# Performance work log

Hardware: AMD Instinct MI355X
Metric: run time of the kernel (lower is better)

## Reference

```python
import jax, jax.numpy as jnp
import numpy as np

B, IN, H, OUT, N = 2048, 512, 512, 256, 32768

def setup_inputs() -> dict:
    key = jax.random.key(0)
    ks = jax.random.split(key, 12)
    s = 1.0 / np.sqrt(H)
    inp = {
        'x': jax.random.normal(ks[0], (B, IN), jnp.float32),
        'Wih0': jax.random.uniform(ks[1], (3 * H, IN), jnp.float32, -s, s),
        'Whh0': jax.random.uniform(ks[2], (3 * H, H), jnp.float32, -s, s),
        'bih0': jax.random.uniform(ks[3], (3 * H,), jnp.float32, -s, s),
        'bhh0': jax.random.uniform(ks[4], (3 * H,), jnp.float32, -s, s),
        'Wih1': jax.random.uniform(ks[5], (3 * H, H), jnp.float32, -s, s),
        'Whh1': jax.random.uniform(ks[6], (3 * H, H), jnp.float32, -s, s),
        'bih1': jax.random.uniform(ks[7], (3 * H,), jnp.float32, -s, s),
        'bhh1': jax.random.uniform(ks[8], (3 * H,), jnp.float32, -s, s),
        'Wout': jax.random.uniform(ks[9], (OUT, H), jnp.float32, -s, s),
        'bout': jax.random.uniform(ks[10], (OUT,), jnp.float32, -s, s),
        'pre_set_idx': jnp.sort(jax.random.randint(ks[11], (N,), 0, B)),
    }
    return inp


def _gru_layer(seq, Wih, Whh, bih, bhh):
    # seq: [B, T, D]; PyTorch GRU gate order: r, z, n
    h_dim = Whh.shape[1]
    xp = jnp.einsum('btd,gd->btg', seq, Wih) + bih  # [B, T, 3H]
    xr, xz, xn = jnp.split(xp, 3, axis=-1)
    Whr, Whz, Whn = jnp.split(Whh, 3, axis=0)
    bhr, bhz, bhn = jnp.split(bhh, 3)

    def step(h, xs):
        xr_t, xz_t, xn_t = xs
        r = jax.nn.sigmoid(xr_t + h @ Whr.T + bhr)
        z = jax.nn.sigmoid(xz_t + h @ Whz.T + bhz)
        n = jnp.tanh(xn_t + r * (h @ Whn.T + bhn))
        h_new = (1.0 - z) * n + z * h
        return h_new, h_new

    h0 = jnp.zeros((seq.shape[0], h_dim), seq.dtype)
    xs = (xr.transpose(1, 0, 2), xz.transpose(1, 0, 2), xn.transpose(1, 0, 2))
    _, ys = jax.lax.scan(step, h0, xs)  # ys: [T, B, H]
    return ys.transpose(1, 0, 2)


def reference(x, Wih0, Whh0, bih0, bhh0, Wih1, Whh1, bih1, bhh1, Wout, bout, pre_set_idx):
    psi_np = np.asarray(pre_set_idx)
    counts_np = np.bincount(psi_np, minlength=B)
    T = int(counts_np.max())  # scipy mode(...).count == max count (static w.r.t. seed)

    # replicate the single-step input T times (original cat loop)
    x_seq = jnp.broadcast_to(x[:, None, :], (B, T, x.shape[1]))
    y0 = _gru_layer(x_seq, Wih0, Whh0, bih0, bhh0)
    y1 = _gru_layer(y0, Wih1, Whh1, bih1, bhh1)  # [B, T, H]

    # masked gather: for batch i, keep first cnt[i] timesteps (pre_set_idx is sorted)
    counts = jnp.asarray(counts_np)
    starts = jnp.concatenate([jnp.zeros(1, counts.dtype), jnp.cumsum(counts)[:-1]])
    rank = jnp.arange(N) - starts[pre_set_idx]  # position within each group
    gather_idx = pre_set_idx * T + rank
    flat = y1.reshape(-1, H)  # [B*T, H]
    sel = flat[gather_idx]  # [N, H]
    return sel @ Wout.T + bout  # [N, OUT]
```

## Files before the change

### kernel.cpp

```cpp
#include <hip/hip_runtime.h>
#include <math.h>

#define Bn   2048
#define Hd   512
#define H3   1536
#define OUTD 256
#define Nn   32768
#define TMAX 48
#define Kd   512

typedef __attribute__((ext_vector_type(8))) short short8v;
typedef __attribute__((ext_vector_type(4))) float float4v;

__device__ __forceinline__ float sigm(float x) { return 1.0f / (1.0f + __expf(-x)); }

__device__ __forceinline__ short f2bf(float v) {
    union { float f; unsigned u; } a; a.f = v;
    unsigned r = a.u + 0x7fffu + ((a.u >> 16) & 1u);
    return (short)(r >> 16);
}
__device__ __forceinline__ float bf2f(short s) {
    union { float f; unsigned u; } a; a.u = ((unsigned)(unsigned short)s) << 16;
    return a.f;
}

#define MF(acc, A, B) acc = __builtin_amdgcn_mfma_f32_16x16x32_bf16(A, B, acc, 0, 0, 0)

__global__ void prologue(const int* __restrict__ psi, int* __restrict__ perm,
                         int* __restrict__ startsP, int* __restrict__ active) {
    __shared__ int hist[64];
    __shared__ int base[64];
    __shared__ int cur[64];
    __shared__ int cnt_s[Bn];
    __shared__ int start_s[Bn];
    const int tid = threadIdx.x;
    if (tid < 64) { hist[tid] = 0; cur[tid] = 0; }
    __syncthreads();
    for (int b = tid; b < Bn; b += 1024) {
        int lo = 0, hi = Nn;
        while (lo < hi) { int mid = (lo + hi) >> 1; if (psi[mid] < b) lo = mid + 1; else hi = mid; }
        int lb = lo;
        lo = 0; hi = Nn;
        while (lo < hi) { int mid = (lo + hi) >> 1; if (psi[mid] <= b) lo = mid + 1; else hi = mid; }
        int c = lo - lb;
        cnt_s[b] = c;
        start_s[b] = lb;
        atomicAdd(&hist[min(c, 63)], 1);
    }
    __syncthreads();
    if (tid == 0) {
        base[63] = 0;
        for (int c = 62; c >= 0; --c) base[c] = base[c + 1] + hist[c + 1];
    }
    __syncthreads();
    if (tid < 64) active[tid] = base[tid];
    for (int b = tid; b < Bn; b += 1024) {
        int c = min(cnt_s[b], 63);
        int pos = base[c] + atomicAdd(&cur[c], 1);
        perm[pos] = b;
        startsP[pos] = start_s[b];
    }
}

__global__ __launch_bounds__(256)
void split_kern(const float* __restrict__ src, short* __restrict__ hi,
                short* __restrict__ lo, int n) {
    int i = (blockIdx.x * 256 + threadIdx.x) * 4;
    if (i >= n) return;
    float4 v = *(const float4*)&src[i];
    float vv[4] = {v.x, v.y, v.z, v.w};
    short h4[4], l4[4];
    #pragma unroll
    for (int c = 0; c < 4; ++c) {
        short h = f2bf(vv[c]);
        h4[c] = h;
        l4[c] = f2bf(vv[c] - bf2f(h));
    }
    *(short4*)&hi[i] = make_short4(h4[0], h4[1], h4[2], h4[3]);
    *(short4*)&lo[i] = make_short4(l4[0], l4[1], l4[2], l4[3]);
}

__global__ __launch_bounds__(256)
void split_perm(const float* __restrict__ src, const int* __restrict__ perm,
                short* __restrict__ hi, short* __restrict__ lo) {
    int i = (blockIdx.x * 256 + threadIdx.x) * 4;
    int row = i >> 9, col = i & 511;
    int srow = perm[row];
    float4 v = *(const float4*)&src[(size_t)srow * 512 + col];
    float vv[4] = {v.x, v.y, v.z, v.w};
    short h4[4], l4[4];
    #pragma unroll
    for (int c = 0; c < 4; ++c) {
        short h = f2bf(vv[c]);
        h4[c] = h;
        l4[c] = f2bf(vv[c] - bf2f(h));
    }
    *(short4*)&hi[i] = make_short4(h4[0], h4[1], h4[2], h4[3]);
    *(short4*)&lo[i] = make_short4(l4[0], l4[1], l4[2], l4[3]);
}

__global__ __launch_bounds__(256)
void pack_w1rz(const float* __restrict__ Wih1, const float* __restrict__ Whh1,
               short* __restrict__ hi, short* __restrict__ lo) {
    int i = (blockIdx.x * 256 + threadIdx.x) * 4;
    int orow = i >> 10, k = i & 1023;
    const float* s = (k < 512) ? &Wih1[(size_t)orow * 512 + k]
                               : &Whh1[(size_t)orow * 512 + (k - 512)];
    float4 v = *(const float4*)s;
    float vv[4] = {v.x, v.y, v.z, v.w};
    short h4[4], l4[4];
    #pragma unroll
    for (int c = 0; c < 4; ++c) {
        short h = f2bf(vv[c]);
        h4[c] = h;
        l4[c] = f2bf(vv[c] - bf2f(h));
    }
    *(short4*)&hi[i] = make_short4(h4[0], h4[1], h4[2], h4[3]);
    *(short4*)&lo[i] = make_short4(l4[0], l4[1], l4[2], l4[3]);
}

__global__ __launch_bounds__(256)
void zero4(short* __restrict__ a, short* __restrict__ b,
           short* __restrict__ c, short* __restrict__ d, int n) {
    int i = (blockIdx.x * 256 + threadIdx.x) * 4;
    if (i >= n) return;
    short4 z = make_short4(0, 0, 0, 0);
    *(short4*)&a[i] = z; *(short4*)&b[i] = z;
    *(short4*)&c[i] = z; *(short4*)&d[i] = z;
}

template<bool SPLIT_A>
__device__ __forceinline__ void gemm_tile(
    const short* __restrict__ Ahi, const short* __restrict__ Alo,
    const short* __restrict__ Whi, const short* __restrict__ Wlo,
    const float* __restrict__ bias, float* __restrict__ C,
    int m0, int n0, int ldC, short* lds) {
    short* ldsAhi = lds;
    short* ldsAlo = lds + 4096;
    short* ldsBhi = lds + 8192;
    short* ldsBlo = lds + 12288;
    const int tid = threadIdx.x;
    const int wid = tid >> 6, lane = tid & 63;
    const int wm = wid >> 1, wn = wid & 1;
    const int oi0 = tid * 2, oi1 = tid * 2 + 1;
    const int r0 = oi0 >> 2, c0 = oi0 & 3;
    const int r1 = oi1 >> 2, c1 = oi1 & 3;
    const int w0 = ((r0 >> 4) * 64 + (r0 & 15) + (c0 << 4)) * 8;
    const int w1 = ((r1 >> 4) * 64 + (r1 & 15) + (c1 << 4)) * 8;

    float4v acc[4][4] = {};
    int4 ah0, ah1, al0, al1, bh0, bh1, bl0, bl1;

#define LOADK(kt) do { const int k0 = (kt) * 32; \
    ah0 = *(const int4*)&Ahi[(size_t)(m0 + r0) * Kd + k0 + c0 * 8]; \
    ah1 = *(const int4*)&Ahi[(size_t)(m0 + r1) * Kd + k0 + c1 * 8]; \
    if constexpr (SPLIT_A) { \
        al0 = *(const int4*)&Alo[(size_t)(m0 + r0) * Kd + k0 + c0 * 8]; \
        al1 = *(const int4*)&Alo[(size_t)(m0 + r1) * Kd + k0 + c1 * 8]; } \
    bh0 = *(const int4*)&Whi[(size_t)(n0 + r0) * Kd + k0 + c0 * 8]; \
    bh1 = *(const int4*)&Whi[(size_t)(n0 + r1) * Kd + k0 + c1 * 8]; \
    bl0 = *(const int4*)&Wlo[(size_t)(n0 + r0) * Kd + k0 + c0 * 8]; \
    bl1 = *(const int4*)&Wlo[(size_t)(n0 + r1) * Kd + k0 + c1 * 8]; } while (0)

    LOADK(0);
    for (int kt = 0; kt < 16; ++kt) {
        __syncthreads();
        *(int4*)&ldsAhi[w0] = ah0; *(int4*)&ldsAhi[w1] = ah1;
        if constexpr (SPLIT_A) { *(int4*)&ldsAlo[w0] = al0; *(int4*)&ldsAlo[w1] = al1; }
        *(int4*)&ldsBhi[w0] = bh0; *(int4*)&ldsBhi[w1] = bh1;
        *(int4*)&ldsBlo[w0] = bl0; *(int4*)&ldsBlo[w1] = bl1;
        __syncthreads();
        if (kt < 15) LOADK(kt + 1);
        short8v afh[4], afl[4], bfh[4], bfl[4];
        #pragma unroll
        for (int mi = 0; mi < 4; ++mi) {
            afh[mi] = *(const short8v*)&ldsAhi[((wm * 4 + mi) * 64 + lane) * 8];
            if constexpr (SPLIT_A)
                afl[mi] = *(const short8v*)&ldsAlo[((wm * 4 + mi) * 64 + lane) * 8];
        }
        #pragma unroll
        for (int ni = 0; ni < 4; ++ni) {
            bfh[ni] = *(const short8v*)&ldsBhi[((wn * 4 + ni) * 64 + lane) * 8];
            bfl[ni] = *(const short8v*)&ldsBlo[((wn * 4 + ni) * 64 + lane) * 8];
        }
        #pragma unroll
        for (int mi = 0; mi < 4; ++mi)
            #pragma unroll
            for (int ni = 0; ni < 4; ++ni) {
                MF(acc[mi][ni], afh[mi], bfh[ni]);
                MF(acc[mi][ni], afh[mi], bfl[ni]);
                if constexpr (SPLIT_A) MF(acc[mi][ni], afl[mi], bfh[ni]);
            }
    }
#undef LOADK
    #pragma unroll
    for (int mi = 0; mi < 4; ++mi) {
        #pragma unroll
        for (int ni = 0; ni < 4; ++ni) {
            int row = m0 + wm * 64 + mi * 16 + ((lane >> 4) << 2);
            int col = n0 + wn * 64 + ni * 16 + (lane & 15);
            float bv = bias ? bias[col] : 0.0f;
            #pragma unroll
            for (int r = 0; r < 4; ++r)
                C[(size_t)(row + r) * ldC + col] = acc[mi][ni][r] + bv;
        }
    }
}

template<bool SPLIT_A>
__global__ __launch_bounds__(256)
void gemm_one(const short* __restrict__ Ahi, const short* __restrict__ Alo,
              const short* __restrict__ Whi, const short* __restrict__ Wlo,
              const float* __restrict__ bias, float* __restrict__ C, int ntn) {
    __shared__ short lds[16384];
    int m0 = (blockIdx.x / ntn) * 128, n0 = (blockIdx.x % ntn) * 128;
    gemm_tile<SPLIT_A>(Ahi, Alo, Whi, Wlo, bias, C, m0, n0, ntn * 128, lds);
}

__global__ __launch_bounds__(256)
void fused_step(const short* __restrict__ OLDhi, const short* __restrict__ OLDlo,
                short* __restrict__ NEWhi, short* __restrict__ NEWlo,
                const short* __restrict__ W0hi, const short* __restrict__ W0lo,
                const short* __restrict__ Wrzhi, const short* __restrict__ Wrzlo,
                const short* __restrict__ Wnxhi, const short* __restrict__ Wnxlo,
                const short* __restrict__ Wnhhi, const short* __restrict__ Wnhlo,
                const float* __restrict__ xp0P, const float* __restrict__ bhh0,
                const float* __restrict__ bih1, const float* __restrict__ bhh1,
                short* __restrict__ sel_h, const int* __restrict__ startsP,
                const int* __restrict__ active, int i) {
    __shared__ short lds[14336];
    const int tid = threadIdx.x;
    const int bb = blockIdx.x;
    const int part = (bb >= 256);
    const int idx = bb & 255;
    const int js = idx >> 4, mb = idx & 15;
    const int m0 = mb * 128, j0 = js * 32;
    const int wid = tid >> 6, lane = tid & 63;
    const int wm = wid >> 1, wn = wid & 1;

    short* ldsAhi = lds;
    short* ldsAlo = lds + 4096;
    short* ldsP   = lds + 8192;

    const int oiA0 = tid * 2, oiA1 = tid * 2 + 1;
    const int rA0 = oiA0 >> 2, cA0 = oiA0 & 3;
    const int rA1 = oiA1 >> 2, cA1 = oiA1 & 3;
    const int wA0 = ((rA0 >> 4) * 64 + (rA0 & 15) + (cA0 << 4)) * 8;
    const int wA1 = ((rA1 >> 4) * 64 + (rA1 & 15) + (cA1 << 4)) * 8;

    const short* aB0h = OLDhi + (size_t)(m0 + rA0) * 1024 + cA0 * 8;
    const short* aB1h = OLDhi + (size_t)(m0 + rA1) * 1024 + cA1 * 8;
    const short* aB0l = OLDlo + (size_t)(m0 + rA0) * 1024 + cA0 * 8;
    const short* aB1l = OLDlo + (size_t)(m0 + rA1) * 1024 + cA1 * 8;

    int wPq[3], pg[3], prw[3], poc[3];
    #pragma unroll
    for (int rep = 0; rep < 3; ++rep) {
        int id2 = rep * 256 + tid;
        int p = id2 >> 7, wi = id2 & 127;
        int prow = wi >> 2, poct = wi & 3;
        wPq[rep] = p * 1024 + ((prow >> 4) * 64 + (prow & 15) + (poct << 4)) * 8;
        pg[rep] = p; prw[rep] = prow; poc[rep] = poct;
    }

    const int col = j0 + wn * 16 + (lane & 15);

#define AFRAGS \
    short8v afh[4], afl[4]; \
    _Pragma("unroll") for (int mi = 0; mi < 4; ++mi) { \
        afh[mi] = *(const short8v*)&ldsAhi[((wm * 4 + mi) * 64 + lane) * 8]; \
        afl[mi] = *(const short8v*)&ldsAlo[((wm * 4 + mi) * 64 + lane) * 8]; }

#define GATEB(ACC, G) { \
    short8v bh = *(const short8v*)&ldsP[((G) * 2 + 0) * 1024 + (wn * 64 + lane) * 8]; \
    short8v bl = *(const short8v*)&ldsP[((G) * 2 + 1) * 1024 + (wn * 64 + lane) * 8]; \
    _Pragma("unroll") for (int mi = 0; mi < 4; ++mi) { \
        MF(ACC[mi], afh[mi], bh); MF(ACC[mi], afh[mi], bl); MF(ACC[mi], afl[mi], bh); } }

    if (part == 0) {
        const int act = active[i];
        if (m0 >= act) return;
        const short* pb[3];
        #pragma unroll
        for (int rep = 0; rep < 3; ++rep) {
            const short* W = (pg[rep] & 1) ? W0lo : W0hi;
            pb[rep] = W + (size_t)((pg[rep] >> 1) * 512 + j0 + prw[rep]) * 512 + poc[rep] * 8;
        }
        float4v aR[4] = {}, aZ[4] = {}, aN[4] = {};
        int4 s0, s1, s2, s3, q0, q1, q2;
        auto LOAD = [&](int kt) {
            int k0 = kt * 32;
            s0 = *(const int4*)(aB0h + k0); s1 = *(const int4*)(aB1h + k0);
            s2 = *(const int4*)(aB0l + k0); s3 = *(const int4*)(aB1l + k0);
            q0 = *(const int4*)(pb[0] + k0);
            q1 = *(const int4*)(pb[1] + k0);
            q2 = *(const int4*)(pb[2] + k0);
        };
        LOAD(0);
        for (int kt = 0; kt < 16; ++kt) {
            __syncthreads();
            *(int4*)&ldsAhi[wA0] = s0; *(int4*)&ldsAhi[wA1] = s1;
            *(int4*)&ldsAlo[wA0] = s2; *(int4*)&ldsAlo[wA1] = s3;
            *(int4*)&ldsP[wPq[0]] = q0; *(int4*)&ldsP[wPq[1]] = q1; *(int4*)&ldsP[wPq[2]] = q2;
            __syncthreads();
            if (kt < 15) LOAD(kt + 1);
            AFRAGS
            GATEB(aR, 0)
            GATEB(aZ, 1)
            GATEB(aN, 2)
        }
        const float b_r = bhh0[col], b_z = bhh0[512 + col], b_n = bhh0[1024 + col];
        #pragma unroll
        for (int mi = 0; mi < 4; ++mi) {
            int rowb = m0 + wm * 64 + mi * 16 + ((lane >> 4) << 2);
            #pragma unroll
            for (int r = 0; r < 4; ++r) {
                int row = rowb + r;
                float xr = xp0P[(size_t)row * H3 + col];
                float xz = xp0P[(size_t)row * H3 + 512 + col];
                float xn = xp0P[(size_t)row * H3 + 1024 + col];
                float rr = sigm(xr + aR[mi][r] + b_r);
                float zz = sigm(xz + aZ[mi][r] + b_z);
                float nn = tanhf(xn + rr * (aN[mi][r] + b_n));
                float hp = bf2f(OLDhi[(size_t)row * 1024 + col]) + bf2f(OLDlo[(size_t)row * 1024 + col]);
                float h = (1.0f - zz) * nn + zz * hp;
                short hh = f2bf(h);
                NEWhi[(size_t)row * 1024 + col] = hh;
                NEWlo[(size_t)row * 1024 + col] = f2bf(h - bf2f(hh));
            }
        }
    } else {
        if (i < 1) return;
        const int act = active[i - 1];
        if (m0 >= act) return;
        const int t = i - 1;
        const short* pbRZ[3]; const short* pbNx[3]; const short* pbNh[3]; int isn[3];
        #pragma unroll
        for (int rep = 0; rep < 3; ++rep) {
            int g = pg[rep] >> 1, hl = pg[rep] & 1;
            isn[rep] = (g == 2);
            const short* Wrz = hl ? Wrzlo : Wrzhi;
            const short* Wx  = hl ? Wnxlo : Wnxhi;
            const short* Wh  = hl ? Wnhlo : Wnhhi;
            pbRZ[rep] = Wrz + (size_t)(min(g, 1) * 512 + j0 + prw[rep]) * 1024 + poc[rep] * 8;
            pbNx[rep] = Wx + (size_t)(j0 + prw[rep]) * 512 + poc[rep] * 8;
            pbNh[rep] = Wh + (size_t)(j0 + prw[rep]) * 512 + poc[rep] * 8;
        }
        float4v aR[4] = {}, aZ[4] = {}, aXn[4] = {}, aHn[4] = {};
        int4 s0, s1, s2, s3, q0, q1, q2;
        auto LOAD = [&](int kt) {
            int k0 = kt * 32;
            s0 = *(const int4*)(aB0h + k0); s1 = *(const int4*)(aB1h + k0);
            s2 = *(const int4*)(aB0l + k0); s3 = *(const int4*)(aB1l + k0);
            q0 = *(const int4*)(isn[0] ? ((kt < 16) ? pbNx[0] + k0 : pbNh[0] + (k0 - 512)) : pbRZ[0] + k0);
            q1 = *(const int4*)(isn[1] ? ((kt < 16) ? pbNx[1] + k0 : pbNh[1] + (k0 - 512)) : pbRZ[1] + k0);
            q2 = *(const int4*)(isn[2] ? ((kt < 16) ? pbNx[2] + k0 : pbNh[2] + (k0 - 512)) : pbRZ[2] + k0);
        };
        LOAD(0);
        for (int kt = 0; kt < 16; ++kt) {
            __syncthreads();
            *(int4*)&ldsAhi[wA0] = s0; *(int4*)&ldsAhi[wA1] = s1;
            *(int4*)&ldsAlo[wA0] = s2; *(int4*)&ldsAlo[wA1] = s3;
            *(int4*)&ldsP[wPq[0]] = q0; *(int4*)&ldsP[wPq[1]] = q1; *(int4*)&ldsP[wPq[2]] = q2;
            __syncthreads();
            LOAD(kt + 1);
            AFRAGS
            GATEB(aR, 0)
            GATEB(aZ, 1)
            GATEB(aXn, 2)
        }
        for (int kt = 16; kt < 32; ++kt) {
            __syncthreads();
            *(int4*)&ldsAhi[wA0] = s0; *(int4*)&ldsAhi[wA1] = s1;
            *(int4*)&ldsAlo[wA0] = s2; *(int4*)&ldsAlo[wA1] = s3;
            *(int4*)&ldsP[wPq[0]] = q0; *(int4*)&ldsP[wPq[1]] = q1; *(int4*)&ldsP[wPq[2]] = q2;
            __syncthreads();
            if (kt < 31) LOAD(kt + 1);
            AFRAGS
            GATEB(aR, 0)
            GATEB(aZ, 1)
            GATEB(aHn, 2)
        }
        const float b_r = bih1[col] + bhh1[col];
        const float b_z = bih1[512 + col] + bhh1[512 + col];
        const float b_xn = bih1[1024 + col];
        const float b_hn = bhh1[1024 + col];
        #pragma unroll
        for (int mi = 0; mi < 4; ++mi) {
            int rowb = m0 + wm * 64 + mi * 16 + ((lane >> 4) << 2);
            #pragma unroll
            for (int r = 0; r < 4; ++r) {
                int row = rowb + r;
                float rr = sigm(aR[mi][r] + b_r);
                float zz = sigm(aZ[mi][r] + b_z);
                float nn = tanhf(aXn[mi][r] + b_xn + rr * (aHn[mi][r] + b_hn));
                float hp = bf2f(OLDhi[(size_t)row * 1024 + 512 + col]) + bf2f(OLDlo[(size_t)row * 1024 + 512 + col]);
                float h = (1.0f - zz) * nn + zz * hp;
                short hh = f2bf(h);
                NEWhi[(size_t)row * 1024 + 512 + col] = hh;
                NEWlo[(size_t)row * 1024 + 512 + col] = f2bf(h - bf2f(hh));
                if (row < act)
                    sel_h[((size_t)startsP[row] + t) * Hd + col] = f2bf(h);
            }
        }
    }
#undef AFRAGS
#undef GATEB
}

extern "C" void kernel_launch(void* const* d_in, const int* in_sizes, int n_in,
                              void* d_out, int out_size, void* d_ws, size_t ws_size,
                              hipStream_t stream) {
    (void)in_sizes; (void)n_in; (void)out_size; (void)ws_size;
    const float* x    = (const float*)d_in[0];
    const float* Wih0 = (const float*)d_in[1];
    const float* Whh0 = (const float*)d_in[2];
    const float* bih0 = (const float*)d_in[3];
    const float* bhh0 = (const float*)d_in[4];
    const float* Wih1 = (const float*)d_in[5];
    const float* Whh1 = (const float*)d_in[6];
    const float* bih1 = (const float*)d_in[7];
    const float* bhh1 = (const float*)d_in[8];
    const float* Wout = (const float*)d_in[9];
    const float* bout = (const float*)d_in[10];
    const int*   psi  = (const int*)d_in[11];
    float* out = (float*)d_out;

    char* p = (char*)d_ws;
    auto alloc = [&](size_t bytes) { char* r = p; p += (bytes + 255) & ~255ULL; return r; };
    short* xPhi   = (short*)alloc((size_t)Bn * Kd * 2);
    short* xPlo   = (short*)alloc((size_t)Bn * Kd * 2);
    short* Wih0hi = (short*)alloc((size_t)H3 * Kd * 2);
    short* Wih0lo = (short*)alloc((size_t)H3 * Kd * 2);
    short* W0hi   = (short*)alloc((size_t)H3 * Kd * 2);
    short* W0lo   = (short*)alloc((size_t)H3 * Kd * 2);
    short* Wrzhi  = (short*)alloc((size_t)1024 * 1024 * 2);
    short* Wrzlo  = (short*)alloc((size_t)1024 * 1024 * 2);
    short* Wnxhi  = (short*)alloc((size_t)512 * 512 * 2);
    short* Wnxlo  = (short*)alloc((size_t)512 * 512 * 2);
    short* Wnhhi  = (short*)alloc((size_t)512 * 512 * 2);
    short* Wnhlo  = (short*)alloc((size_t)512 * 512 * 2);
    short* Wouthi = (short*)alloc((size_t)OUTD * Kd * 2);
    short* Woutlo = (short*)alloc((size_t)OUTD * Kd * 2);
    float* xp0P   = (float*)alloc((size_t)Bn * H3 * 4);
    short* Aahi   = (short*)alloc((size_t)Bn * 1024 * 2);
    short* Aalo   = (short*)alloc((size_t)Bn * 1024 * 2);
    short* Abhi   = (short*)alloc((size_t)Bn * 1024 * 2);
    short* Ablo   = (short*)alloc((size_t)Bn * 1024 * 2);
    short* sel_h  = (short*)alloc((size_t)Nn * Hd * 2);
    int* perm     = (int*)alloc(Bn * 4);
    int* startsP  = (int*)alloc(Bn * 4);
    int* active   = (int*)alloc(64 * 4);

    prologue<<<1, 1024, 0, stream>>>(psi, perm, startsP, active);
    split_perm<<<1024, 256, 0, stream>>>(x, perm, xPhi, xPlo);
    split_kern<<<768, 256, 0, stream>>>(Wih0, Wih0hi, Wih0lo, H3 * Kd);
    split_kern<<<768, 256, 0, stream>>>(Whh0, W0hi, W0lo, H3 * Kd);
    pack_w1rz<<<1024, 256, 0, stream>>>(Wih1, Whh1, Wrzhi, Wrzlo);
    split_kern<<<256, 256, 0, stream>>>(Wih1 + (size_t)1024 * 512, Wnxhi, Wnxlo, 512 * 512);
    split_kern<<<256, 256, 0, stream>>>(Whh1 + (size_t)1024 * 512, Wnhhi, Wnhlo, 512 * 512);
    split_kern<<<128, 256, 0, stream>>>(Wout, Wouthi, Woutlo, OUTD * Kd);
    zero4<<<2048, 256, 0, stream>>>(Aahi, Aalo, Abhi, Ablo, Bn * 1024);

    gemm_one<true><<<192, 256, 0, stream>>>(xPhi, xPlo, Wih0hi, Wih0lo, bih0, xp0P, 12);

    for (int i = 0; i <= TMAX; ++i) {
        const short* OLDhi = (i & 1) ? Abhi : Aahi;
        const short* OLDlo = (i & 1) ? Ablo : Aalo;
        short* NEWhi = (i & 1) ? Aahi : Abhi;
        short* NEWlo = (i & 1) ? Aalo : Ablo;
        fused_step<<<512, 256, 0, stream>>>(OLDhi, OLDlo, NEWhi, NEWlo,
                                            W0hi, W0lo, Wrzhi, Wrzlo,
                                            Wnxhi, Wnxlo, Wnhhi, Wnhlo,
                                            xp0P, bhh0, bih1, bhh1,
                                            sel_h, startsP, active, i);
    }

    gemm_one<false><<<512, 256, 0, stream>>>(sel_h, nullptr, Wouthi, Woutlo, bout, out, 2);
}
```

Before: 1.766 ms.

## Rebalance fused GRU step tiles: wider layer-0 N tiles, smaller layer-1 M tiles

Layer-0 blocks now compute 128x64 output tiles (128 blocks) instead of 128x32 (256 blocks), which halves redundant reloads of the hidden-state A tile. Layer-1 blocks use 64x64 tiles (256 blocks), so the longer K=1024 work is split across more blocks and the two layers are better balanced. The grid drops from 512 to 384 blocks, LDS grows to 40KB, and launch bounds request 2 blocks per CU. This trades per-block register pressure and LDS use for less redundant global loading and better load balance.

Result: slower. 4.008 ms (+127.0%).

```diff
diff --git a/kernel.cpp b/kernel.cpp
--- a/kernel.cpp
+++ b/kernel.cpp
@@ -217,7 +217,7 @@
     gemm_tile<SPLIT_A>(Ahi, Alo, Whi, Wlo, bias, C, m0, n0, ntn * 128, lds);
 }
 
-__global__ __launch_bounds__(256)
+__global__ __launch_bounds__(256, 2)
 void fused_step(const short* __restrict__ OLDhi, const short* __restrict__ OLDlo,
                 short* __restrict__ NEWhi, short* __restrict__ NEWlo,
                 const short* __restrict__ W0hi, const short* __restrict__ W0lo,
@@ -228,184 +228,218 @@
                 const float* __restrict__ bih1, const float* __restrict__ bhh1,
                 short* __restrict__ sel_h, const int* __restrict__ startsP,
                 const int* __restrict__ active, int i) {
-    __shared__ short lds[14336];
+    __shared__ short lds[20480];
+    short* ldsA = lds;
+    short* ldsP = lds + 8192;
     const int tid = threadIdx.x;
     const int bb = blockIdx.x;
-    const int part = (bb >= 256);
-    const int idx = bb & 255;
-    const int js = idx >> 4, mb = idx & 15;
-    const int m0 = mb * 128, j0 = js * 32;
     const int wid = tid >> 6, lane = tid & 63;
     const int wm = wid >> 1, wn = wid & 1;
 
-    short* ldsAhi = lds;
-    short* ldsAlo = lds + 4096;
-    short* ldsP   = lds + 8192;
-
-    const int oiA0 = tid * 2, oiA1 = tid * 2 + 1;
-    const int rA0 = oiA0 >> 2, cA0 = oiA0 & 3;
-    const int rA1 = oiA1 >> 2, cA1 = oiA1 & 3;
-    const int wA0 = ((rA0 >> 4) * 64 + (rA0 & 15) + (cA0 << 4)) * 8;
-    const int wA1 = ((rA1 >> 4) * 64 + (rA1 & 15) + (cA1 << 4)) * 8;
-
-    const short* aB0h = OLDhi + (size_t)(m0 + rA0) * 1024 + cA0 * 8;
-    const short* aB1h = OLDhi + (size_t)(m0 + rA1) * 1024 + cA1 * 8;
-    const short* aB0l = OLDlo + (size_t)(m0 + rA0) * 1024 + cA0 * 8;
-    const short* aB1l = OLDlo + (size_t)(m0 + rA1) * 1024 + cA1 * 8;
-
-    int wPq[3], pg[3], prw[3], poc[3];
-    #pragma unroll
-    for (int rep = 0; rep < 3; ++rep) {
-        int id2 = rep * 256 + tid;
-        int p = id2 >> 7, wi = id2 & 127;
-        int prow = wi >> 2, poct = wi & 3;
-        wPq[rep] = p * 1024 + ((prow >> 4) * 64 + (prow & 15) + (poct << 4)) * 8;
-        pg[rep] = p; prw[rep] = prow; poc[rep] = poct;
-    }
-
-    const int col = j0 + wn * 16 + (lane & 15);
-
-#define AFRAGS \
-    short8v afh[4], afl[4]; \
-    _Pragma("unroll") for (int mi = 0; mi < 4; ++mi) { \
-        afh[mi] = *(const short8v*)&ldsAhi[((wm * 4 + mi) * 64 + lane) * 8]; \
-        afl[mi] = *(const short8v*)&ldsAlo[((wm * 4 + mi) * 64 + lane) * 8]; }
-
-#define GATEB(ACC, G) { \
-    short8v bh = *(const short8v*)&ldsP[((G) * 2 + 0) * 1024 + (wn * 64 + lane) * 8]; \
-    short8v bl = *(const short8v*)&ldsP[((G) * 2 + 1) * 1024 + (wn * 64 + lane) * 8]; \
-    _Pragma("unroll") for (int mi = 0; mi < 4; ++mi) { \
-        MF(ACC[mi], afh[mi], bh); MF(ACC[mi], afh[mi], bl); MF(ACC[mi], afl[mi], bh); } }
-
-    if (part == 0) {
+    if (bb < 128) {
         const int act = active[i];
+        const int mb = bb >> 3, js = bb & 7;
+        const int m0 = mb * 128, j0 = js * 64;
         if (m0 >= act) return;
-        const short* pb[3];
-        #pragma unroll
-        for (int rep = 0; rep < 3; ++rep) {
-            const short* W = (pg[rep] & 1) ? W0lo : W0hi;
-            pb[rep] = W + (size_t)((pg[rep] >> 1) * 512 + j0 + prw[rep]) * 512 + poc[rep] * 8;
-        }
-        float4v aR[4] = {}, aZ[4] = {}, aN[4] = {};
-        int4 s0, s1, s2, s3, q0, q1, q2;
+
+        int aOff[4]; const short* aSrc[4];
+        #pragma unroll
+        for (int rep = 0; rep < 4; ++rep) {
+            int u = rep * 256 + tid;
+            int half = u >> 9, wi = u & 511;
+            int ar = wi >> 2, ac = wi & 3;
+            aOff[rep] = half * 4096 + ((ar >> 4) * 64 + (ar & 15) + (ac << 4)) * 8;
+            aSrc[rep] = (half ? OLDlo : OLDhi) + (size_t)(m0 + ar) * 1024 + ac * 8;
+        }
+        int pOff[6]; const short* pSrc[6];
+        #pragma unroll
+        for (int rep = 0; rep < 6; ++rep) {
+            int u = rep * 256 + tid;
+            int p = u >> 8, wi = u & 255;
+            int pr = wi >> 2, pc = wi & 3;
+            pOff[rep] = p * 2048 + ((pr >> 4) * 64 + (pr & 15) + (pc << 4)) * 8;
+            int g = p >> 1, hl = p & 1;
+            pSrc[rep] = (hl ? W0lo : W0hi) + (size_t)(g * 512 + j0 + pr) * 512 + pc * 8;
+        }
+
+        float4v aR[4][2] = {}, aZ[4][2] = {}, aN[4][2] = {};
+        int4 av[4], pv[6];
         auto LOAD = [&](int kt) {
-            int k0 = kt * 32;
-            s0 = *(const int4*)(aB0h + k0); s1 = *(const int4*)(aB1h + k0);
-            s2 = *(const int4*)(aB0l + k0); s3 = *(const int4*)(aB1l + k0);
-            q0 = *(const int4*)(pb[0] + k0);
-            q1 = *(const int4*)(pb[1] + k0);
-            q2 = *(const int4*)(pb[2] + k0);
+            const int k0 = kt * 32;
+            #pragma unroll
+            for (int rep = 0; rep < 4; ++rep) av[rep] = *(const int4*)(aSrc[rep] + k0);
+            #pragma unroll
+            for (int rep = 0; rep < 6; ++rep) pv[rep] = *(const int4*)(pSrc[rep] + k0);
         };
         LOAD(0);
         for (int kt = 0; kt < 16; ++kt) {
             __syncthreads();
-            *(int4*)&ldsAhi[wA0] = s0; *(int4*)&ldsAhi[wA1] = s1;
-            *(int4*)&ldsAlo[wA0] = s2; *(int4*)&ldsAlo[wA1] = s3;
-            *(int4*)&ldsP[wPq[0]] = q0; *(int4*)&ldsP[wPq[1]] = q1; *(int4*)&ldsP[wPq[2]] = q2;
+            #pragma unroll
+            for (int rep = 0; rep < 4; ++rep) *(int4*)&ldsA[aOff[rep]] = av[rep];
+            #pragma unroll
+            for (int rep = 0; rep < 6; ++rep) *(int4*)&ldsP[pOff[rep]] = pv[rep];
             __syncthreads();
             if (kt < 15) LOAD(kt + 1);
-            AFRAGS
-            GATEB(aR, 0)
-            GATEB(aZ, 1)
-            GATEB(aN, 2)
-        }
-        const float b_r = bhh0[col], b_z = bhh0[512 + col], b_n = bhh0[1024 + col];
-        #pragma unroll
-        for (int mi = 0; mi < 4; ++mi) {
-            int rowb = m0 + wm * 64 + mi * 16 + ((lane >> 4) << 2);
-            #pragma unroll
-            for (int r = 0; r < 4; ++r) {
-                int row = rowb + r;
-                float xr = xp0P[(size_t)row * H3 + col];
-                float xz = xp0P[(size_t)row * H3 + 512 + col];
-                float xn = xp0P[(size_t)row * H3 + 1024 + col];
-                float rr = sigm(xr + aR[mi][r] + b_r);
-                float zz = sigm(xz + aZ[mi][r] + b_z);
-                float nn = tanhf(xn + rr * (aN[mi][r] + b_n));
-                float hp = bf2f(OLDhi[(size_t)row * 1024 + col]) + bf2f(OLDlo[(size_t)row * 1024 + col]);
-                float h = (1.0f - zz) * nn + zz * hp;
-                short hh = f2bf(h);
-                NEWhi[(size_t)row * 1024 + col] = hh;
-                NEWlo[(size_t)row * 1024 + col] = f2bf(h - bf2f(hh));
+            short8v afh[4], afl[4];
+            #pragma unroll
+            for (int mi = 0; mi < 4; ++mi) {
+                afh[mi] = *(const short8v*)&ldsA[((wm * 4 + mi) * 64 + lane) * 8];
+                afl[mi] = *(const short8v*)&ldsA[4096 + ((wm * 4 + mi) * 64 + lane) * 8];
+            }
+            #pragma unroll
+            for (int ni = 0; ni < 2; ++ni) {
+                {   short8v bh = *(const short8v*)&ldsP[0 * 2048 + ((wn * 2 + ni) * 64 + lane) * 8];
+                    short8v bl = *(const short8v*)&ldsP[1 * 2048 + ((wn * 2 + ni) * 64 + lane) * 8];
+                    #pragma unroll
+                    for (int mi = 0; mi < 4; ++mi) { MF(aR[mi][ni], afh[mi], bh); MF(aR[mi][ni], afh[mi], bl); MF(aR[mi][ni], afl[mi], bh); } }
+                {   short8v bh = *(const short8v*)&ldsP[2 * 2048 + ((wn * 2 + ni) * 64 + lane) * 8];
+                    short8v bl = *(const short8v*)&ldsP[3 * 2048 + ((wn * 2 + ni) * 64 + lane) * 8];
+                    #pragma unroll
+                    for (int mi = 0; mi < 4; ++mi) { MF(aZ[mi][ni], afh[mi], bh); MF(aZ[mi][ni], afh[mi], bl); MF(aZ[mi][ni], afl[mi], bh); } }
+                {   short8v bh = *(const short8v*)&ldsP[4 * 2048 + ((wn * 2 + ni) * 64 + lane) * 8];
+                    short8v bl = *(const short8v*)&ldsP[5 * 2048 + ((wn * 2 + ni) * 64 + lane) * 8];
+                    #pragma unroll
+                    for (int mi = 0; mi < 4; ++mi) { MF(aN[mi][ni], afh[mi], bh); MF(aN[mi][ni], afh[mi], bl); MF(aN[mi][ni], afl[mi], bh); } }
+            }
+        }
+        #pragma unroll
+        for (int ni = 0; ni < 2; ++ni) {
+            const int col = j0 + wn * 32 + ni * 16 + (lane & 15);
+            const float b_r = bhh0[col], b_z = bhh0[512 + col], b_n = bhh0[1024 + col];
+            #pragma unroll
+            for (int mi = 0; mi < 4; ++mi) {
+                int rowb = m0 + wm * 64 + mi * 16 + ((lane >> 4) << 2);
+                #pragma unroll
+                for (int r = 0; r < 4; ++r) {
+                    int row = rowb + r;
+                    float xr = xp0P[(size_t)row * H3 + col];
+                    float xz = xp0P[(size_t)row * H3 + 512 + col];
+                    float xn = xp0P[(size_t)row * H3 + 1024 + col];
+                    float rr = sigm(xr + aR[mi][ni][r] + b_r);
+                    float zz = sigm(xz + aZ[mi][ni][r] + b_z);
+                    float nn = tanhf(xn + rr * (aN[mi][ni][r] + b_n));
+                    float hp = bf2f(OLDhi[(size_t)row * 1024 + col]) + bf2f(OLDlo[(size_t)row * 1024 + col]);
+                    float h = (1.0f - zz) * nn + zz * hp;
+                    short hh = f2bf(h);
+                    NEWhi[(size_t)row * 1024 + col] = hh;
+                    NEWlo[(size_t)row * 1024 + col] = f2bf(h - bf2f(hh));
+                }
             }
         }
     } else {
         if (i < 1) return;
         const int act = active[i - 1];
+        const int idx = bb - 128;
+        const int mb = idx >> 3, js = idx & 7;
+        const int m0 = mb * 64, j0 = js * 64;
         if (m0 >= act) return;
         const int t = i - 1;
-        const short* pbRZ[3]; const short* pbNx[3]; const short* pbNh[3]; int isn[3];
-        #pragma unroll
-        for (int rep = 0; rep < 3; ++rep) {
-            int g = pg[rep] >> 1, hl = pg[rep] & 1;
-            isn[rep] = (g == 2);
+
+        int aOff[2]; const short* aSrc[2];
+        #pragma unroll
+        for (int rep = 0; rep < 2; ++rep) {
+            int u = rep * 256 + tid;
+            int half = u >> 8, wi = u & 255;
+            int ar = wi >> 2, ac = wi & 3;
+            aOff[rep] = half * 4096 + ((ar >> 4) * 64 + (ar & 15) + (ac << 4)) * 8;
+            aSrc[rep] = (half ? OLDlo : OLDhi) + (size_t)(m0 + ar) * 1024 + ac * 8;
+        }
+        int pOff[6]; const short* pA[6]; const short* pB[6];
+        #pragma unroll
+        for (int rep = 0; rep < 6; ++rep) {
+            int u = rep * 256 + tid;
+            int p = u >> 8, wi = u & 255;
+            int pr = wi >> 2, pc = wi & 3;
+            pOff[rep] = p * 2048 + ((pr >> 4) * 64 + (pr & 15) + (pc << 4)) * 8;
+            int g = p >> 1, hl = p & 1;
             const short* Wrz = hl ? Wrzlo : Wrzhi;
             const short* Wx  = hl ? Wnxlo : Wnxhi;
             const short* Wh  = hl ? Wnhlo : Wnhhi;
-            pbRZ[rep] = Wrz + (size_t)(min(g, 1) * 512 + j0 + prw[rep]) * 1024 + poc[rep] * 8;
-            pbNx[rep] = Wx + (size_t)(j0 + prw[rep]) * 512 + poc[rep] * 8;
-            pbNh[rep] = Wh + (size_t)(j0 + prw[rep]) * 512 + poc[rep] * 8;
-        }
-        float4v aR[4] = {}, aZ[4] = {}, aXn[4] = {}, aHn[4] = {};
-        int4 s0, s1, s2, s3, q0, q1, q2;
-        auto LOAD = [&](int kt) {
-            int k0 = kt * 32;
-            s0 = *(const int4*)(aB0h + k0); s1 = *(const int4*)(aB1h + k0);
-            s2 = *(const int4*)(aB0l + k0); s3 = *(const int4*)(aB1l + k0);
-            q0 = *(const int4*)(isn[0] ? ((kt < 16) ? pbNx[0] + k0 : pbNh[0] + (k0 - 512)) : pbRZ[0] + k0);
-            q1 = *(const int4*)(isn[1] ? ((kt < 16) ? pbNx[1] + k0 : pbNh[1] + (k0 - 512)) : pbRZ[1] + k0);
-            q2 = *(const int4*)(isn[2] ? ((kt < 16) ? pbNx[2] + k0 : pbNh[2] + (k0 - 512)) : pbRZ[2] + k0);
+            const short* rz = Wrz + (size_t)(min(g, 1) * 512 + j0 + pr) * 1024 + pc * 8;
+            pA[rep] = (g < 2) ? rz : (Wx + (size_t)(j0 + pr) * 512 + pc * 8);
+            pB[rep] = (g < 2) ? rz : (Wh + (size_t)(j0 + pr) * 512 + pc * 8 - 512);
+        }
+
+        float4v aR[2][2] = {}, aZ[2][2] = {}, aXn[2][2] = {}, aHn[2][2] = {};
+        int4 av[2], pv[6];
+        auto LOAD1 = [&](int kt) {
+            const int k0 = kt * 32;
+            #pragma unroll
+            for (int rep = 0; rep < 2; ++rep) av[rep] = *(const int4*)(aSrc[rep] + k0);
+            #pragma unroll
+            for (int rep = 0; rep < 6; ++rep) pv[rep] = *(const int4*)(pA[rep] + k0);
         };
-        LOAD(0);
+        auto LOAD2 = [&](int kt) {
+            const int k0 = kt * 32;
+            #pragma unroll
+            for (int rep = 0; rep < 2; ++rep) av[rep] = *(const int4*)(aSrc[rep] + k0);
+            #pragma unroll
+            for (int rep = 0; rep < 6; ++rep) pv[rep] = *(const int4*)(pB[rep] + k0);
+        };
+
+#define STAGE() do { \
+    __syncthreads(); \
+    _Pragma("unroll") for (int rep = 0; rep < 2; ++rep) *(int4*)&ldsA[aOff[rep]] = av[rep]; \
+    _Pragma("unroll") for (int rep = 0; rep < 6; ++rep) *(int4*)&ldsP[pOff[rep]] = pv[rep]; \
+    __syncthreads(); } while (0)
+
+#define AFR \
+    short8v afh[2], afl[2]; \
+    _Pragma("unroll") for (int mi = 0; mi < 2; ++mi) { \
+        afh[mi] = *(const short8v*)&ldsA[((wm * 2 + mi) * 64 + lane) * 8]; \
+        afl[mi] = *(const short8v*)&ldsA[4096 + ((wm * 2 + mi) * 64 + lane) * 8]; }
+
+#define GB(ACC, P) { \
+    short8v bh = *(const short8v*)&ldsP[(P) * 4096 + ((wn * 2 + ni) * 64 + lane) * 8]; \
+    short8v bl = *(const short8v*)&ldsP[(P) * 4096 + 2048 + ((wn * 2 + ni) * 64 + lane) * 8]; \
+    _Pragma("unroll") for (int mi = 0; mi < 2; ++mi) { \
+        MF(ACC[mi][ni], afh[mi], bh); MF(ACC[mi][ni], afh[mi], bl); MF(ACC[mi][ni], afl[mi], bh); } }
+
+        LOAD1(0);
         for (int kt = 0; kt < 16; ++kt) {
-            __syncthreads();
-            *(int4*)&ldsAhi[wA0] = s0; *(int4*)&ldsAhi[wA1] = s1;
-            *(int4*)&ldsAlo[wA0] = s2; *(int4*)&ldsAlo[wA1] = s3;
-            *(int4*)&ldsP[wPq[0]] = q0; *(int4*)&ldsP[wPq[1]] = q1; *(int4*)&ldsP[wPq[2]] = q2;
-            __syncthreads();
-            LOAD(kt + 1);
-            AFRAGS
-            GATEB(aR, 0)
-            GATEB(aZ, 1)
-            GATEB(aXn, 2)
+            STAGE();
+            if (kt < 15) LOAD1(kt + 1); else LOAD2(16);
+            AFR
+            #pragma unroll
+            for (int ni = 0; ni < 2; ++ni) { GB(aR, 0) GB(aZ, 1) GB(aXn, 2) }
         }
         for (int kt = 16; kt < 32; ++kt) {
-            __syncthreads();
-            *(int4*)&ldsAhi[wA0] = s0; *(int4*)&ldsAhi[wA1] = s1;
-            *(int4*)&ldsAlo[wA0] = s2; *(int4*)&ldsAlo[wA1] = s3;
-            *(int4*)&ldsP[wPq[0]] = q0; *(int4*)&ldsP[wPq[1]] = q1; *(int4*)&ldsP[wPq[2]] = q2;
-            __syncthreads();
-            if (kt < 31) LOAD(kt + 1);
-            AFRAGS
-            GATEB(aR, 0)
-            GATEB(aZ, 1)
-            GATEB(aHn, 2)
-        }
-        const float b_r = bih1[col] + bhh1[col];
-        const float b_z = bih1[512 + col] + bhh1[512 + col];
-        const float b_xn = bih1[1024 + col];
-        const float b_hn = bhh1[1024 + col];
-        #pragma unroll
-        for (int mi = 0; mi < 4; ++mi) {
-            int rowb = m0 + wm * 64 + mi * 16 + ((lane >> 4) << 2);
-            #pragma unroll
-            for (int r = 0; r < 4; ++r) {
-                int row = rowb + r;
-                float rr = sigm(aR[mi][r] + b_r);
-                float zz = sigm(aZ[mi][r] + b_z);
-                float nn = tanhf(aXn[mi][r] + b_xn + rr * (aHn[mi][r] + b_hn));
-                float hp = bf2f(OLDhi[(size_t)row * 1024 + 512 + col]) + bf2f(OLDlo[(size_t)row * 1024 + 512 + col]);
-                float h = (1.0f - zz) * nn + zz * hp;
-                short hh = f2bf(h);
-                NEWhi[(size_t)row * 1024 + 512 + col] = hh;
-                NEWlo[(size_t)row * 1024 + 512 + col] = f2bf(h - bf2f(hh));
-                if (row < act)
-                    sel_h[((size_t)startsP[row] + t) * Hd + col] = f2bf(h);
+            STAGE();
+            if (kt < 31) LOAD2(kt + 1);
+            AFR
+            #pragma unroll
+            for (int ni = 0; ni < 2; ++ni) { GB(aR, 0) GB(aZ, 1) GB(aHn, 2) }
+        }
+#undef STAGE
+#undef AFR
+#undef GB
+        #pragma unroll
+        for (int ni = 0; ni < 2; ++ni) {
+            const int col = j0 + wn * 32 + ni * 16 + (lane & 15);
+            const float b_r = bih1[col] + bhh1[col];
+            const float b_z = bih1[512 + col] + bhh1[512 + col];
+            const float b_xn = bih1[1024 + col];
+            const float b_hn = bhh1[1024 + col];
+            #pragma unroll
+            for (int mi = 0; mi < 2; ++mi) {
+                int rowb = m0 + wm * 32 + mi * 16 + ((lane >> 4) << 2);
+                #pragma unroll
+                for (int r = 0; r < 4; ++r) {
+                    int row = rowb + r;
+                    float rr = sigm(aR[mi][ni][r] + b_r);
+                    float zz = sigm(aZ[mi][ni][r] + b_z);
+                    float nn = tanhf(aXn[mi][ni][r] + b_xn + rr * (aHn[mi][ni][r] + b_hn));
+                    float hp = bf2f(OLDhi[(size_t)row * 1024 + 512 + col]) + bf2f(OLDlo[(size_t)row * 1024 + 512 + col]);
+                    float h = (1.0f - zz) * nn + zz * hp;
+                    short hh = f2bf(h);
+                    NEWhi[(size_t)row * 1024 + 512 + col] = hh;
+                    NEWlo[(size_t)row * 1024 + 512 + col] = f2bf(h - bf2f(hh));
+                    if (row < act)
+                        sel_h[((size_t)startsP[row] + t) * Hd + col] = f2bf(h);
+                }
             }
         }
     }
-#undef AFRAGS
-#undef GATEB
 }
 
 extern "C" void kernel_launch(void* const* d_in, const int* in_sizes, int n_in,
@@ -469,7 +503,7 @@
         const short* OLDlo = (i & 1) ? Ablo : Aalo;
         short* NEWhi = (i & 1) ? Aahi : Abhi;
         short* NEWlo = (i & 1) ? Aalo : Ablo;
-        fused_step<<<512, 256, 0, stream>>>(OLDhi, OLDlo, NEWhi, NEWlo,
+        fused_step<<<384, 256, 0, stream>>>(OLDhi, OLDlo, NEWhi, NEWlo,
                                             W0hi, W0lo, Wrzhi, Wrzlo,
                                             Wnxhi, Wnxlo, Wnhhi, Wnhlo,
                                             xp0P, bhh0, bih1, bhh1,
```
